# Kernel optimization log

Hardware: AMD Instinct MI355X
Metric: run time of the kernel (lower is better)

Reference implementation:

```python
import jax, jax.numpy as jnp
import numpy as np
from jax import lax

B, C, H, W = 8, 64, 128, 128
KS = 3          # kernel size
K = KS * KS     # kernel field = 9
PAD = 1


def conv2d(x, w, b):
    # x: [B,Cin,H,W], w: [Cout,Cin,kh,kw], 'same' 3x3 conv
    y = lax.conv_general_dilated(x, w, window_strides=(1, 1),
                                 padding=((PAD, PAD), (PAD, PAD)),
                                 dimension_numbers=('NCHW', 'OIHW', 'NCHW'))
    return y + b[None, :, None, None]


def modulated_deform_conv(x, offset, mask, weight, bias):
    # x:[B,C,H,W], offset:[B,2K,H,W] (dy,dx per tap), mask:[B,K,H,W]
    Bs, Cin, Hin, Win = x.shape
    off = offset.reshape(Bs, K, 2, Hin, Win)
    ky, kx = jnp.meshgrid(jnp.arange(KS), jnp.arange(KS), indexing='ij')
    ky = ky.reshape(K).astype(x.dtype)   # kernel tap row offsets 0..2
    kx = kx.reshape(K).astype(x.dtype)
    # sampling positions p = p0 + p_k + offset (stride=1, pad=1)
    py = (jnp.arange(Hin, dtype=x.dtype)[None, None, :, None] - PAD
          + ky[None, :, None, None] + off[:, :, 0])            # [B,K,H,W]
    px = (jnp.arange(Win, dtype=x.dtype)[None, None, None, :] - PAD
          + kx[None, :, None, None] + off[:, :, 1])            # [B,K,H,W]

    y0 = jnp.floor(py); x0 = jnp.floor(px)
    ly = py - y0; lx = px - x0                                  # frac parts
    y0i = y0.astype(jnp.int32); x0i = x0.astype(jnp.int32)

    x_flat = x.reshape(Bs, Cin, Hin * Win)

    def gather(iy, ix):
        valid = ((iy >= 0) & (iy < Hin) & (ix >= 0) & (ix < Win))
        flat = (jnp.clip(iy, 0, Hin - 1) * Win + jnp.clip(ix, 0, Win - 1))
        g = jax.vmap(lambda xb, ib: xb[:, ib])(x_flat, flat.reshape(Bs, -1))
        g = g.reshape(Bs, Cin, K, Hin, Win)
        return g * valid[:, None].astype(x.dtype)

    w00 = ((1 - ly) * (1 - lx))[:, None]  # [B,1,K,H,W]
    w01 = ((1 - ly) * lx)[:, None]
    w10 = (ly * (1 - lx))[:, None]
    w11 = (ly * lx)[:, None]

    val = (w00 * gather(y0i, x0i) + w01 * gather(y0i, x0i + 1)
           + w10 * gather(y0i + 1, x0i) + w11 * gather(y0i + 1, x0i + 1))
    val = val * mask[:, None]                                   # modulation
    out = jnp.einsum('ock,bckhw->bohw', weight.reshape(weight.shape[0], Cin, K), val)
    return out + bias[None, :, None, None]


def setup_inputs() -> dict:
    key = jax.random.key(0)
    ks = jax.random.split(key, 7)
    s = 0.05
    return {
        'x': jax.random.normal(ks[0], (B, C, H, W), jnp.float32),
        'w_om': jax.random.normal(ks[1], (3 * K, C, KS, KS), jnp.float32) * s,
        'b_om': jax.random.normal(ks[2], (3 * K,), jnp.float32) * s,
        'w_dc': jax.random.normal(ks[3], (C, C, KS, KS), jnp.float32) * s,
        'b_dc': jax.random.normal(ks[4], (C,), jnp.float32) * s,
        'w_c': jax.random.normal(ks[5], (C, C, KS, KS), jnp.float32) * s,
        'b_c': jax.random.normal(ks[6], (C,), jnp.float32) * s,
    }


def reference(x, w_om, b_om, w_dc, b_dc, w_c, b_c):
    om = conv2d(x, w_om, b_om)                       # [B,3K,H,W]
    offset, mask_raw = om[:, :2 * K], om[:, 2 * K:]
    mask = 2.0 * jax.nn.sigmoid(mask_raw)
    out = modulated_deform_conv(x, offset, mask, w_dc, b_dc)
    act = jnp.where(out > 0, out, 0.2 * out)         # LeakyReLU(0.2)
    return conv2d(act, w_c, b_c) + x
```

## Files before the change

### kernel.cpp

```cpp
#include <hip/hip_runtime.h>
#include <math.h>

#define Bn 8
#define Cn 64
#define Hn 128
#define Wn 128
#define HWn (Hn * Wn)

#define WOM_OFF 0
#define WDC_OFF 18432
#define WC_OFF 55296

typedef __attribute__((ext_vector_type(8))) short short8;
typedef __attribute__((ext_vector_type(4))) float floatx4;

__device__ __forceinline__ float bf2f(short s) {
  return __uint_as_float(((unsigned)(unsigned short)s) << 16);
}
__device__ __forceinline__ short f2bf(float f) {
  unsigned u = __float_as_uint(f);
  u += 0x7fff + ((u >> 16) & 1);
  return (short)(u >> 16);
}

__global__ __launch_bounds__(256) void k_prep_w(
    const float* __restrict__ w_om, const float* __restrict__ w_dc,
    const float* __restrict__ w_c, short* __restrict__ wt) {
  int idx = blockIdx.x * 256 + threadIdx.x;
  if (idx >= 92160) return;
  float v;
  if (idx < WDC_OFF) {
    int e = idx;
    int elem = e & 7, lane = (e >> 3) & 63, mt = (e >> 9) & 1, t = e >> 10;
    int kk = t % 9, cc = t / 9;
    int row = mt * 16 + (lane & 15);
    int cin = cc * 32 + (lane >> 4) * 8 + elem;
    v = (row < 27) ? w_om[(row * 64 + cin) * 9 + kk] : 0.f;
  } else {
    int e = (idx < WC_OFF) ? idx - WDC_OFF : idx - WC_OFF;
    const float* src = (idx < WC_OFF) ? w_dc : w_c;
    int elem = e & 7, lane = (e >> 3) & 63, mt = (e >> 9) & 3, t = e >> 11;
    int kk = t % 9, cc = t / 9;
    int row = mt * 16 + (lane & 15);
    int cin = cc * 32 + (lane >> 4) * 8 + elem;
    v = src[(row * 64 + cin) * 9 + kk];
  }
  wt[idx] = f2bf(v);
}

__global__ __launch_bounds__(256) void k_prep_x(const float* __restrict__ x,
                                                short* __restrict__ xT) {
  __shared__ float tile[64][129];
  const int bid = blockIdx.x;
  const int b = bid & 7, h = bid >> 3;
  const int tid = threadIdx.x;
  const float* xb = x + (size_t)b * 64 * HWn + h * Wn;
  for (int i = tid; i < 8192; i += 256) {
    int c = i >> 7, w = i & 127;
    tile[c][w] = xb[c * HWn + w];
  }
  __syncthreads();
  short* dst = xT + ((size_t)(b * Hn + h) * Wn) * 64;
  for (int i = tid; i < 2048; i += 256) {
    int w = i >> 4, c4 = (i & 15) * 4;
    short4 o;
    o.x = f2bf(tile[c4 + 0][w]);
    o.y = f2bf(tile[c4 + 1][w]);
    o.z = f2bf(tile[c4 + 2][w]);
    o.w = f2bf(tile[c4 + 3][w]);
    *(short4*)(dst + (size_t)w * 64 + c4) = o;
  }
}

__global__ __launch_bounds__(256, 3) void k_omdef(
    const short* __restrict__ xT, const short* __restrict__ wt,
    const float* __restrict__ b_om, const float* __restrict__ b_dc,
    short* __restrict__ actT) {
  __shared__ __attribute__((aligned(16))) short lw[18432];
  __shared__ float som[27 * 66];
  __shared__ unsigned sbw[4 * 576];
  unsigned* sb01 = sbw;
  unsigned* sb23 = sbw + 576;
  unsigned* sw01 = sbw + 1152;
  unsigned* sw23 = sbw + 1728;

  const int bid = blockIdx.x;
  const int b = bid & 7;
  const int r = bid >> 3;
  const int h = r >> 1, w0 = (r & 1) * 64;
  const int tid = threadIdx.x;
  const int wave = tid >> 6, lane = tid & 63, quad = lane >> 4, lr = lane & 15;
  const short* xb = xT + (size_t)b * HWn * 64;
  const int pxl = wave * 16 + lr;
  const int gxp = w0 + pxl;

  floatx4 zf = {0.f, 0.f, 0.f, 0.f};

  {
    const short8* src = (const short8*)(wt + WOM_OFF);
    short8* dst = (short8*)lw;
    for (int i = tid; i < 2304; i += 256) dst[i] = src[i];
  }
  __syncthreads();

  floatx4 aco[2] = {zf, zf};
#pragma unroll 3
  for (int kk = 0; kk < 9; ++kk) {
    int ky = kk / 3, kx = kk - ky * 3;
    int gy = h + ky - 1, gx = gxp + kx - 1;
    bool ok = ((unsigned)gy < (unsigned)Hn) && ((unsigned)gx < (unsigned)Wn);
    int gyc = min(max(gy, 0), Hn - 1), gxc = min(max(gx, 0), Wn - 1);
    const short* rec = xb + (size_t)(gyc * Wn + gxc) * 64 + quad * 8;
#pragma unroll
    for (int cc = 0; cc < 2; ++cc) {
      short8 bf = *(const short8*)(rec + cc * 32);
      if (!ok) bf = (short8){0, 0, 0, 0, 0, 0, 0, 0};
      short8 a0 = *(const short8*)&lw[((cc * 9 + kk) * 2 + 0) * 512 + lane * 8];
      short8 a1 = *(const short8*)&lw[((cc * 9 + kk) * 2 + 1) * 512 + lane * 8];
      aco[0] = __builtin_amdgcn_mfma_f32_16x16x32_bf16(a0, bf, aco[0], 0, 0, 0);
      aco[1] = __builtin_amdgcn_mfma_f32_16x16x32_bf16(a1, bf, aco[1], 0, 0, 0);
    }
  }
#pragma unroll
  for (int mt = 0; mt < 2; ++mt) {
#pragma unroll
    for (int rr = 0; rr < 4; ++rr) {
      int co = mt * 16 + quad * 4 + rr;
      if (co < 27) {
        float v = aco[mt][rr] + b_om[co];
        if (co >= 18) v = 2.f / (1.f + expf(-v));
        som[co * 66 + pxl] = v;
      }
    }
  }
  __syncthreads();

  {
    const short8* src = (const short8*)(wt + WDC_OFF);
    short8* dst = (short8*)lw;
    for (int i = tid; i < 2304; i += 256) dst[i] = src[i];
  }
  for (int pr = tid; pr < 576; pr += 256) {
    int k = pr >> 6, p = pr & 63;
    float offy = som[(2 * k) * 66 + p];
    float offx = som[(2 * k + 1) * 66 + p];
    float m = som[(18 + k) * 66 + p];
    float py = (float)(h - 1 + (k / 3)) + offy;
    float px_ = (float)(w0 + p - 1 + (k % 3)) + offx;
    float fy = floorf(py), fx = floorf(px_);
    float ly = py - fy, lx = px_ - fx;
    int iy0 = (int)fy, ix0 = (int)fx;
    int iy1 = iy0 + 1, ix1 = ix0 + 1;
    bool vy0 = (iy0 >= 0) && (iy0 < Hn);
    bool vy1 = (iy1 >= 0) && (iy1 < Hn);
    bool vx0 = (ix0 >= 0) && (ix0 < Wn);
    bool vx1 = (ix1 >= 0) && (ix1 < Wn);
    unsigned cy0 = (unsigned)min(max(iy0, 0), Hn - 1);
    unsigned cy1 = (unsigned)min(max(iy1, 0), Hn - 1);
    unsigned cx0 = (unsigned)min(max(ix0, 0), Wn - 1);
    unsigned cx1 = (unsigned)min(max(ix1, 0), Wn - 1);
    sb01[pr] = (cy0 * Wn + cx0) | ((cy0 * Wn + cx1) << 16);
    sb23[pr] = (cy1 * Wn + cx0) | ((cy1 * Wn + cx1) << 16);
    float u0 = (vy0 && vx0) ? (1.f - ly) * (1.f - lx) * m : 0.f;
    float u1 = (vy0 && vx1) ? (1.f - ly) * lx * m : 0.f;
    float u2 = (vy1 && vx0) ? ly * (1.f - lx) * m : 0.f;
    float u3 = (vy1 && vx1) ? ly * lx * m : 0.f;
    sw01[pr] = (unsigned)(unsigned short)f2bf(u0) |
               ((unsigned)(unsigned short)f2bf(u1) << 16);
    sw23[pr] = (unsigned)(unsigned short)f2bf(u2) |
               ((unsigned)(unsigned short)f2bf(u3) << 16);
  }
  __syncthreads();

  floatx4 acc[4] = {zf, zf, zf, zf};
  for (int cc = 0; cc < 2; ++cc) {
    if (cc) {
      __syncthreads();
      const short8* src = (const short8*)(wt + WDC_OFF + 18432);
      short8* dst = (short8*)lw;
      for (int i = tid; i < 2304; i += 256) dst[i] = src[i];
      __syncthreads();
    }
#pragma unroll 3
    for (int kk = 0; kk < 9; ++kk) {
      int pr = kk * 64 + pxl;
      unsigned a01 = sb01[pr], a23 = sb23[pr];
      unsigned uw01 = sw01[pr], uw23 = sw23[pr];
      float u0 = bf2f((short)(uw01 & 0xFFFF));
      float u1 = bf2f((short)(uw01 >> 16));
      float u2 = bf2f((short)(uw23 & 0xFFFF));
      float u3 = bf2f((short)(uw23 >> 16));
      int co = cc * 32 + quad * 8;
      short8 q0 = *(const short8*)(xb + (size_t)(a01 & 0xFFFF) * 64 + co);
      short8 q1 = *(const short8*)(xb + (size_t)(a01 >> 16) * 64 + co);
      short8 q2 = *(const short8*)(xb + (size_t)(a23 & 0xFFFF) * 64 + co);
      short8 q3 = *(const short8*)(xb + (size_t)(a23 >> 16) * 64 + co);
      short8 bf;
#pragma unroll
      for (int e = 0; e < 8; ++e) {
        float f = u0 * bf2f(q0[e]) + u1 * bf2f(q1[e]) + u2 * bf2f(q2[e]) +
                  u3 * bf2f(q3[e]);
        bf[e] = f2bf(f);
      }
#pragma unroll
      for (int mt = 0; mt < 4; ++mt) {
        short8 am = *(const short8*)&lw[(kk * 4 + mt) * 512 + lane * 8];
        acc[mt] = __builtin_amdgcn_mfma_f32_16x16x32_bf16(am, bf, acc[mt], 0, 0, 0);
      }
    }
  }

  short* ab = actT + ((size_t)(b * Hn + h) * Wn + w0) * 64;
#pragma unroll
  for (int mt = 0; mt < 4; ++mt) {
    int c0 = mt * 16 + quad * 4;
    short4 o;
    float v;
    v = acc[mt][0] + b_dc[c0 + 0]; o.x = f2bf(v > 0.f ? v : 0.2f * v);
    v = acc[mt][1] + b_dc[c0 + 1]; o.y = f2bf(v > 0.f ? v : 0.2f * v);
    v = acc[mt][2] + b_dc[c0 + 2]; o.z = f2bf(v > 0.f ? v : 0.2f * v);
    v = acc[mt][3] + b_dc[c0 + 3]; o.w = f2bf(v > 0.f ? v : 0.2f * v);
    *(short4*)(ab + (size_t)pxl * 64 + c0) = o;
  }
}

__global__ __launch_bounds__(256, 4) void k_conv_out(
    const short* __restrict__ actT, const short* __restrict__ wt,
    const float* __restrict__ b_c, const float* __restrict__ x,
    float* __restrict__ out) {
  __shared__ __attribute__((aligned(16))) short lw[18432];

  const int bid = blockIdx.x;
  const int b = bid & 7;
  const int r = bid >> 3;
  const int h = r >> 1, w0 = (r & 1) * 64;
  const int tid = threadIdx.x;
  const int wave = tid >> 6, lane = tid & 63, quad = lane >> 4, lr = lane & 15;
  const short* ab = actT + (size_t)b * HWn * 64;
  const int pxl = wave * 16 + lr;
  const int gxp = w0 + pxl;

  floatx4 zf = {0.f, 0.f, 0.f, 0.f};
  floatx4 acc[4] = {zf, zf, zf, zf};

  for (int cc = 0; cc < 2; ++cc) {
    if (cc) __syncthreads();
    {
      const short8* src = (const short8*)(wt + WC_OFF + cc * 18432);
      short8* dst = (short8*)lw;
      for (int i = tid; i < 2304; i += 256) dst[i] = src[i];
    }
    __syncthreads();
#pragma unroll 3
    for (int kk = 0; kk < 9; ++kk) {
      int ky = kk / 3, kx = kk - ky * 3;
      int gy = h + ky - 1, gx = gxp + kx - 1;
      bool ok = ((unsigned)gy < (unsigned)Hn) && ((unsigned)gx < (unsigned)Wn);
      int gyc = min(max(gy, 0), Hn - 1), gxc = min(max(gx, 0), Wn - 1);
      short8 bf = *(const short8*)(ab + (size_t)(gyc * Wn + gxc) * 64 +
                                   cc * 32 + quad * 8);
      if (!ok) bf = (short8){0, 0, 0, 0, 0, 0, 0, 0};
#pragma unroll
      for (int mt = 0; mt < 4; ++mt) {
        short8 am = *(const short8*)&lw[(kk * 4 + mt) * 512 + lane * 8];
        acc[mt] = __builtin_amdgcn_mfma_f32_16x16x32_bf16(am, bf, acc[mt], 0, 0, 0);
      }
    }
  }
  __syncthreads();

  float* ot = (float*)lw;
#pragma unroll
  for (int mt = 0; mt < 4; ++mt) {
#pragma unroll
    for (int rr = 0; rr < 4; ++rr) {
      ot[(mt * 16 + quad * 4 + rr) * 66 + pxl] = acc[mt][rr];
    }
  }
  __syncthreads();

  const int row = tid >> 2, seg = tid & 3;
  const float bias = b_c[row];
  const size_t gbase = ((size_t)(b * 64 + row) * Hn + h) * Wn + w0 + seg * 16;
  const float* xr = x + gbase;
  float* op = out + gbase;
#pragma unroll
  for (int j = 0; j < 4; ++j) {
    floatx4 t = *(const floatx4*)&ot[row * 66 + seg * 16 + j * 4];
    floatx4 xv = *(const floatx4*)&xr[j * 4];
    t = t + xv;
    t[0] += bias; t[1] += bias; t[2] += bias; t[3] += bias;
    *(floatx4*)&op[j * 4] = t;
  }
}

extern "C" void kernel_launch(void* const* d_in, const int* in_sizes, int n_in,
                              void* d_out, int out_size, void* d_ws,
                              size_t ws_size, hipStream_t stream) {
  const float* x = (const float*)d_in[0];
  const float* w_om = (const float*)d_in[1];
  const float* b_om = (const float*)d_in[2];
  const float* w_dc = (const float*)d_in[3];
  const float* b_dc = (const float*)d_in[4];
  const float* w_c = (const float*)d_in[5];
  const float* b_c = (const float*)d_in[6];
  float* out = (float*)d_out;

  short* xT = (short*)d_ws;
  short* actT = xT + (size_t)Bn * HWn * 64;
  short* wt = actT + (size_t)Bn * HWn * 64;

  k_prep_w<<<dim3(360), 256, 0, stream>>>(w_om, w_dc, w_c, wt);
  k_prep_x<<<dim3(1024), 256, 0, stream>>>(x, xT);
  k_omdef<<<dim3(2048), 256, 0, stream>>>(xT, wt, b_om, b_dc, actT);
  k_conv_out<<<dim3(2048), 256, 0, stream>>>(actT, wt, b_c, x, out);
}
```

Measured before the change: 231.0 us.

## Read MFMA weight fragments straight from global memory instead of staging in LDS

Both the offset/deform kernel and the output conv kernel stop copying their 36 KB weight slices into shared memory. Each wave now loads its MFMA A-operand fragments directly from global memory and relies on L1/L2 caching. This removes the cooperative copies and several block barriers, and the smaller shared footprint allows raising the occupancy hint to 5 blocks. In exchange, every wave issues redundant global loads for the same weights, adding cache traffic and latency to the MFMA loop.

```diff
diff --git a/kernel.cpp b/kernel.cpp
--- a/kernel.cpp
+++ b/kernel.cpp
@@ -72,11 +72,10 @@
   }
 }
 
-__global__ __launch_bounds__(256, 3) void k_omdef(
+__global__ __launch_bounds__(256, 5) void k_omdef(
     const short* __restrict__ xT, const short* __restrict__ wt,
     const float* __restrict__ b_om, const float* __restrict__ b_dc,
     short* __restrict__ actT) {
-  __shared__ __attribute__((aligned(16))) short lw[18432];
   __shared__ float som[27 * 66];
   __shared__ unsigned sbw[4 * 576];
   unsigned* sb01 = sbw;
@@ -96,13 +95,6 @@
 
   floatx4 zf = {0.f, 0.f, 0.f, 0.f};
 
-  {
-    const short8* src = (const short8*)(wt + WOM_OFF);
-    short8* dst = (short8*)lw;
-    for (int i = tid; i < 2304; i += 256) dst[i] = src[i];
-  }
-  __syncthreads();
-
   floatx4 aco[2] = {zf, zf};
 #pragma unroll 3
   for (int kk = 0; kk < 9; ++kk) {
@@ -115,8 +107,10 @@
     for (int cc = 0; cc < 2; ++cc) {
       short8 bf = *(const short8*)(rec + cc * 32);
       if (!ok) bf = (short8){0, 0, 0, 0, 0, 0, 0, 0};
-      short8 a0 = *(const short8*)&lw[((cc * 9 + kk) * 2 + 0) * 512 + lane * 8];
-      short8 a1 = *(const short8*)&lw[((cc * 9 + kk) * 2 + 1) * 512 + lane * 8];
+      short8 a0 = *(const short8*)(wt + WOM_OFF +
+                                   ((cc * 9 + kk) * 2 + 0) * 512 + lane * 8);
+      short8 a1 = *(const short8*)(wt + WOM_OFF +
+                                   ((cc * 9 + kk) * 2 + 1) * 512 + lane * 8);
       aco[0] = __builtin_amdgcn_mfma_f32_16x16x32_bf16(a0, bf, aco[0], 0, 0, 0);
       aco[1] = __builtin_amdgcn_mfma_f32_16x16x32_bf16(a1, bf, aco[1], 0, 0, 0);
     }
@@ -135,11 +129,6 @@
   }
   __syncthreads();
 
-  {
-    const short8* src = (const short8*)(wt + WDC_OFF);
-    short8* dst = (short8*)lw;
-    for (int i = tid; i < 2304; i += 256) dst[i] = src[i];
-  }
   for (int pr = tid; pr < 576; pr += 256) {
     int k = pr >> 6, p = pr & 63;
     float offy = som[(2 * k) * 66 + p];
@@ -173,14 +162,9 @@
   __syncthreads();
 
   floatx4 acc[4] = {zf, zf, zf, zf};
+#pragma unroll
   for (int cc = 0; cc < 2; ++cc) {
-    if (cc) {
-      __syncthreads();
-      const short8* src = (const short8*)(wt + WDC_OFF + 18432);
-      short8* dst = (short8*)lw;
-      for (int i = tid; i < 2304; i += 256) dst[i] = src[i];
-      __syncthreads();
-    }
+    const short* wbase = wt + WDC_OFF + cc * 18432;
 #pragma unroll 3
     for (int kk = 0; kk < 9; ++kk) {
       int pr = kk * 64 + pxl;
@@ -204,7 +188,7 @@
       }
 #pragma unroll
       for (int mt = 0; mt < 4; ++mt) {
-        short8 am = *(const short8*)&lw[(kk * 4 + mt) * 512 + lane * 8];
+        short8 am = *(const short8*)(wbase + (kk * 4 + mt) * 512 + lane * 8);
         acc[mt] = __builtin_amdgcn_mfma_f32_16x16x32_bf16(am, bf, acc[mt], 0, 0, 0);
       }
     }
@@ -224,11 +208,11 @@
   }
 }
 
-__global__ __launch_bounds__(256, 4) void k_conv_out(
+__global__ __launch_bounds__(256, 5) void k_conv_out(
     const short* __restrict__ actT, const short* __restrict__ wt,
     const float* __restrict__ b_c, const float* __restrict__ x,
     float* __restrict__ out) {
-  __shared__ __attribute__((aligned(16))) short lw[18432];
+  __shared__ __attribute__((aligned(16))) float ot[64 * 66];
 
   const int bid = blockIdx.x;
   const int b = bid & 7;
@@ -243,14 +227,9 @@
   floatx4 zf = {0.f, 0.f, 0.f, 0.f};
   floatx4 acc[4] = {zf, zf, zf, zf};
 
+#pragma unroll
   for (int cc = 0; cc < 2; ++cc) {
-    if (cc) __syncthreads();
-    {
-      const short8* src = (const short8*)(wt + WC_OFF + cc * 18432);
-      short8* dst = (short8*)lw;
-      for (int i = tid; i < 2304; i += 256) dst[i] = src[i];
-    }
-    __syncthreads();
+    const short* wbase = wt + WC_OFF + cc * 18432;
 #pragma unroll 3
     for (int kk = 0; kk < 9; ++kk) {
       int ky = kk / 3, kx = kk - ky * 3;
@@ -262,14 +241,12 @@
       if (!ok) bf = (short8){0, 0, 0, 0, 0, 0, 0, 0};
 #pragma unroll
       for (int mt = 0; mt < 4; ++mt) {
-        short8 am = *(const short8*)&lw[(kk * 4 + mt) * 512 + lane * 8];
+        short8 am = *(const short8*)(wbase + (kk * 4 + mt) * 512 + lane * 8);
         acc[mt] = __builtin_amdgcn_mfma_f32_16x16x32_bf16(am, bf, acc[mt], 0, 0, 0);
       }
     }
   }
-  __syncthreads();
-
-  float* ot = (float*)lw;
+
 #pragma unroll
   for (int mt = 0; mt < 4; ++mt) {
 #pragma unroll
```

Result: slower. 256.3 us (+10.9%).

## Split fused offset/mask conv and deformable sampling into two kernels

Applied to the files above, without the earlier changes.

The fused offset-conv plus deformable-conv kernel is split into k_om, which computes offsets and masks and writes packed bilinear indices and weights to a global workspace, and k_def, which reads them and does the gather and MFMA. k_om now reads its weights directly from global memory instead of staging them in LDS. Each kernel uses less LDS and declares a higher launch bound, which is meant to raise occupancy. The cost is an extra launch and a global round-trip for the 2048x2304-word parameter buffer (about 19 MB).

```diff
diff --git a/kernel.cpp b/kernel.cpp
--- a/kernel.cpp
+++ b/kernel.cpp
@@ -13,6 +13,7 @@
 
 typedef __attribute__((ext_vector_type(8))) short short8;
 typedef __attribute__((ext_vector_type(4))) float floatx4;
+typedef __attribute__((ext_vector_type(4))) unsigned uintx4;
 
 __device__ __forceinline__ float bf2f(short s) {
   return __uint_as_float(((unsigned)(unsigned short)s) << 16);
@@ -72,17 +73,10 @@
   }
 }
 
-__global__ __launch_bounds__(256, 3) void k_omdef(
+__global__ __launch_bounds__(256, 4) void k_om(
     const short* __restrict__ xT, const short* __restrict__ wt,
-    const float* __restrict__ b_om, const float* __restrict__ b_dc,
-    short* __restrict__ actT) {
-  __shared__ __attribute__((aligned(16))) short lw[18432];
+    const float* __restrict__ b_om, unsigned* __restrict__ params) {
   __shared__ float som[27 * 66];
-  __shared__ unsigned sbw[4 * 576];
-  unsigned* sb01 = sbw;
-  unsigned* sb23 = sbw + 576;
-  unsigned* sw01 = sbw + 1152;
-  unsigned* sw23 = sbw + 1728;
 
   const int bid = blockIdx.x;
   const int b = bid & 7;
@@ -95,14 +89,6 @@
   const int gxp = w0 + pxl;
 
   floatx4 zf = {0.f, 0.f, 0.f, 0.f};
-
-  {
-    const short8* src = (const short8*)(wt + WOM_OFF);
-    short8* dst = (short8*)lw;
-    for (int i = tid; i < 2304; i += 256) dst[i] = src[i];
-  }
-  __syncthreads();
-
   floatx4 aco[2] = {zf, zf};
 #pragma unroll 3
   for (int kk = 0; kk < 9; ++kk) {
@@ -115,8 +101,10 @@
     for (int cc = 0; cc < 2; ++cc) {
       short8 bf = *(const short8*)(rec + cc * 32);
       if (!ok) bf = (short8){0, 0, 0, 0, 0, 0, 0, 0};
-      short8 a0 = *(const short8*)&lw[((cc * 9 + kk) * 2 + 0) * 512 + lane * 8];
-      short8 a1 = *(const short8*)&lw[((cc * 9 + kk) * 2 + 1) * 512 + lane * 8];
+      short8 a0 = *(const short8*)(wt + WOM_OFF +
+                                   ((cc * 9 + kk) * 2 + 0) * 512 + lane * 8);
+      short8 a1 = *(const short8*)(wt + WOM_OFF +
+                                   ((cc * 9 + kk) * 2 + 1) * 512 + lane * 8);
       aco[0] = __builtin_amdgcn_mfma_f32_16x16x32_bf16(a0, bf, aco[0], 0, 0, 0);
       aco[1] = __builtin_amdgcn_mfma_f32_16x16x32_bf16(a1, bf, aco[1], 0, 0, 0);
     }
@@ -135,11 +123,7 @@
   }
   __syncthreads();
 
-  {
-    const short8* src = (const short8*)(wt + WDC_OFF);
-    short8* dst = (short8*)lw;
-    for (int i = tid; i < 2304; i += 256) dst[i] = src[i];
-  }
+  unsigned* pb = params + (size_t)bid * 2304;
   for (int pr = tid; pr < 576; pr += 256) {
     int k = pr >> 6, p = pr & 63;
     float offy = som[(2 * k) * 66 + p];
@@ -159,37 +143,57 @@
     unsigned cy1 = (unsigned)min(max(iy1, 0), Hn - 1);
     unsigned cx0 = (unsigned)min(max(ix0, 0), Wn - 1);
     unsigned cx1 = (unsigned)min(max(ix1, 0), Wn - 1);
-    sb01[pr] = (cy0 * Wn + cx0) | ((cy0 * Wn + cx1) << 16);
-    sb23[pr] = (cy1 * Wn + cx0) | ((cy1 * Wn + cx1) << 16);
     float u0 = (vy0 && vx0) ? (1.f - ly) * (1.f - lx) * m : 0.f;
     float u1 = (vy0 && vx1) ? (1.f - ly) * lx * m : 0.f;
     float u2 = (vy1 && vx0) ? ly * (1.f - lx) * m : 0.f;
     float u3 = (vy1 && vx1) ? ly * lx * m : 0.f;
-    sw01[pr] = (unsigned)(unsigned short)f2bf(u0) |
-               ((unsigned)(unsigned short)f2bf(u1) << 16);
-    sw23[pr] = (unsigned)(unsigned short)f2bf(u2) |
-               ((unsigned)(unsigned short)f2bf(u3) << 16);
-  }
-  __syncthreads();
-
+    uintx4 pk;
+    pk.x = (cy0 * Wn + cx0) | ((cy0 * Wn + cx1) << 16);
+    pk.y = (cy1 * Wn + cx0) | ((cy1 * Wn + cx1) << 16);
+    pk.z = (unsigned)(unsigned short)f2bf(u0) |
+           ((unsigned)(unsigned short)f2bf(u1) << 16);
+    pk.w = (unsigned)(unsigned short)f2bf(u2) |
+           ((unsigned)(unsigned short)f2bf(u3) << 16);
+    *(uintx4*)(pb + (size_t)pr * 4) = pk;
+  }
+}
+
+__global__ __launch_bounds__(256, 4) void k_def(
+    const short* __restrict__ xT, const short* __restrict__ wt,
+    const unsigned* __restrict__ params, const float* __restrict__ b_dc,
+    short* __restrict__ actT) {
+  __shared__ __attribute__((aligned(16))) short lw[18432];
+
+  const int bid = blockIdx.x;
+  const int b = bid & 7;
+  const int r = bid >> 3;
+  const int h = r >> 1, w0 = (r & 1) * 64;
+  const int tid = threadIdx.x;
+  const int wave = tid >> 6, lane = tid & 63, quad = lane >> 4, lr = lane & 15;
+  const short* xb = xT + (size_t)b * HWn * 64;
+  const int pxl = wave * 16 + lr;
+  const unsigned* pb = params + (size_t)bid * 2304;
+  (void)h; (void)w0;
+
+  floatx4 zf = {0.f, 0.f, 0.f, 0.f};
   floatx4 acc[4] = {zf, zf, zf, zf};
+
   for (int cc = 0; cc < 2; ++cc) {
-    if (cc) {
-      __syncthreads();
-      const short8* src = (const short8*)(wt + WDC_OFF + 18432);
+    if (cc) __syncthreads();
+    {
+      const short8* src = (const short8*)(wt + WDC_OFF + cc * 18432);
       short8* dst = (short8*)lw;
       for (int i = tid; i < 2304; i += 256) dst[i] = src[i];
-      __syncthreads();
-    }
+    }
+    __syncthreads();
 #pragma unroll 3
     for (int kk = 0; kk < 9; ++kk) {
-      int pr = kk * 64 + pxl;
-      unsigned a01 = sb01[pr], a23 = sb23[pr];
-      unsigned uw01 = sw01[pr], uw23 = sw23[pr];
-      float u0 = bf2f((short)(uw01 & 0xFFFF));
-      float u1 = bf2f((short)(uw01 >> 16));
-      float u2 = bf2f((short)(uw23 & 0xFFFF));
-      float u3 = bf2f((short)(uw23 >> 16));
+      uintx4 p4 = *(const uintx4*)(pb + (size_t)(kk * 64 + pxl) * 4);
+      unsigned a01 = p4.x, a23 = p4.y;
+      float u0 = bf2f((short)(p4.z & 0xFFFF));
+      float u1 = bf2f((short)(p4.z >> 16));
+      float u2 = bf2f((short)(p4.w & 0xFFFF));
+      float u3 = bf2f((short)(p4.w >> 16));
       int co = cc * 32 + quad * 8;
       short8 q0 = *(const short8*)(xb + (size_t)(a01 & 0xFFFF) * 64 + co);
       short8 q1 = *(const short8*)(xb + (size_t)(a01 >> 16) * 64 + co);
@@ -210,7 +214,8 @@
     }
   }
 
-  short* ab = actT + ((size_t)(b * Hn + h) * Wn + w0) * 64;
+  const int gr = bid >> 3;
+  short* ab = actT + ((size_t)(b * Hn + (gr >> 1)) * Wn + (gr & 1) * 64) * 64;
 #pragma unroll
   for (int mt = 0; mt < 4; ++mt) {
     int c0 = mt * 16 + quad * 4;
@@ -309,9 +314,11 @@
   short* xT = (short*)d_ws;
   short* actT = xT + (size_t)Bn * HWn * 64;
   short* wt = actT + (size_t)Bn * HWn * 64;
+  unsigned* params = (unsigned*)(wt + 92160);
 
   k_prep_w<<<dim3(360), 256, 0, stream>>>(w_om, w_dc, w_c, wt);
   k_prep_x<<<dim3(1024), 256, 0, stream>>>(x, xT);
-  k_omdef<<<dim3(2048), 256, 0, stream>>>(xT, wt, b_om, b_dc, actT);
+  k_om<<<dim3(2048), 256, 0, stream>>>(xT, wt, b_om, params);
+  k_def<<<dim3(2048), 256, 0, stream>>>(xT, wt, params, b_dc, actT);
   k_conv_out<<<dim3(2048), 256, 0, stream>>>(actT, wt, b_c, x, out);
 }
```

New measurement: 241.3 us. +4.5%, slower.
